# Performance work log

Measured on AMD Instinct MI355X. Metric: run time of the kernel, lower is better.

Reference implementation:

```python
import jax, jax.numpy as jnp
import numpy as np

SQ, SK, B, NP, HN = 2048, 2048, 2, 32, 64

def setup_inputs() -> dict:
    key = jax.random.key(0)
    kq, kk, kv, km = jax.random.split(key, 4)
    query = jax.random.normal(kq, (SQ, B, NP, HN), dtype=jnp.float32)
    k = jax.random.normal(kk, (SK, B, NP, HN), dtype=jnp.float32)
    value = jax.random.normal(kv, (SK, B, NP, HN), dtype=jnp.float32)
    # True = masked position (matches tf.where(mask, -10000.0, scores));
    # use a causal-style mask broadcast over heads.
    causal = ~jnp.tril(jnp.ones((SQ, SK), dtype=bool))  # True above diagonal
    attention_mask = jnp.broadcast_to(causal[None, None], (B, 1, SQ, SK))
    return {"query": query, "key": k, "value": value, "attention_mask": attention_mask}

def reference(query, key, value, attention_mask):
    sq, b, nh, hn = query.shape
    norm_factor = jnp.sqrt(jnp.asarray(hn, dtype=query.dtype))
    # scores: [b, nh, sq, sk]
    scores = jnp.einsum('sbnh,tbnh->bnst', query, key) / norm_factor
    scores = jnp.where(attention_mask, jnp.asarray(-10000.0, scores.dtype), scores)
    probs = jax.nn.softmax(scores, axis=-1)
    # dropout rate is 0.0 / inference -> identity
    # context: [sq, b, nh, hn] -> [sq, b, nh*hn]
    context = jnp.einsum('bnst,tbnh->sbnh', probs, value)
    return context.reshape(sq, b, nh * hn)
```

## Files before the change

### kernel.cpp

```cpp
#include <hip/hip_runtime.h>


typedef __attribute__((ext_vector_type(8))) short frag8;
typedef __attribute__((ext_vector_type(4))) float f32x4;
typedef __attribute__((ext_vector_type(2))) float f32x2;
typedef __attribute__((ext_vector_type(2))) __bf16 bf16x2;

#define SQ_    2048
#define NH_    64
#define HN_    64
#define ROWS_  4096
#define P_P    40
#define VT_P   40
#define TP_    72
#define SC2    (0.125f * 1.44269504088896340736f)
#define MASK2  (-3.0e4f)
#define MINIT  (-1.0e30f)

__device__ __forceinline__ unsigned short f2bf(float f) {
    unsigned u = __float_as_uint(f);
    u += 0x7fffu + ((u >> 16) & 1u);
    return (unsigned short)(u >> 16);
}

__device__ __forceinline__ float fexp2(float x) {
#if __has_builtin(__builtin_amdgcn_exp2f)
    return __builtin_amdgcn_exp2f(x);
#else
    return exp2f(x);
#endif
}

__device__ __forceinline__ unsigned pack_bf16x2(float lo, float hi) {
    bf16x2 h = __builtin_convertvector((f32x2){lo, hi}, bf16x2);
    unsigned r;
    __builtin_memcpy(&r, &h, 4);
    return r;
}

__device__ __forceinline__ frag8 pack8s(const float* __restrict__ p, float s) {
    float4 a = *(const float4*)p;
    float4 b = *(const float4*)(p + 4);
    frag8 r;
    r[0] = (short)f2bf(a.x * s); r[1] = (short)f2bf(a.y * s);
    r[2] = (short)f2bf(a.z * s); r[3] = (short)f2bf(a.w * s);
    r[4] = (short)f2bf(b.x * s); r[5] = (short)f2bf(b.y * s);
    r[6] = (short)f2bf(b.z * s); r[7] = (short)f2bf(b.w * s);
    return r;
}

__device__ __forceinline__ void gll(const void* g, void* l) {
    __builtin_amdgcn_global_load_lds(
        (const __attribute__((address_space(1))) unsigned int*)(uintptr_t)g,
        (__attribute__((address_space(3))) unsigned int*)(unsigned int)(uintptr_t)l,
        16, 0, 0);
}

__global__ void __launch_bounds__(256)
prep_kv(const float* __restrict__ K, const float* __restrict__ V,
        unsigned short* __restrict__ Kh, unsigned short* __restrict__ Vblk)
{
    __shared__ __align__(16) unsigned short tile[HN_ * TP_];
    const int tid = threadIdx.x;
    const int hd  = blockIdx.x & 63;
    const int s0  = (blockIdx.x >> 6) << 6;

    {
        const int c2 = tid & 3;
        const int sl = tid >> 2;
        const int s  = s0 + sl;
        const int sk = s >> 1;
        const float* kp = K + (size_t)s * ROWS_ + hd * HN_ + c2 * 16;
        frag8 A = pack8s(kp, 1.0f);
        frag8 Bf = pack8s(kp + 8, 1.0f);
        unsigned short* kr = Kh + (size_t)hd * (SQ_ * HN_) + (size_t)s * HN_;
        *(frag8*)(kr + ((2 * c2 + sk) & 7) * 8)     = A;
        *(frag8*)(kr + ((2 * c2 + 1 + sk) & 7) * 8) = Bf;
    }

    {
        const int c   = (tid & 15) * 4;
        const int tl0 = tid >> 4;
#pragma unroll
        for (int k = 0; k < 4; ++k) {
            const int tl = tl0 + k * 16;
            float4 v = *(const float4*)(V + (size_t)(s0 + tl) * ROWS_ + hd * HN_ + c);
            tile[(c + 0) * TP_ + tl] = f2bf(v.x);
            tile[(c + 1) * TP_ + tl] = f2bf(v.y);
            tile[(c + 2) * TP_ + tl] = f2bf(v.z);
            tile[(c + 3) * TP_ + tl] = f2bf(v.w);
        }
    }
    __syncthreads();
    {
        const int u  = tid & 3;
        const int dd = tid >> 2;
        const int rv = (dd + (dd >> 1)) & 3;
#pragma unroll
        for (int tb = 0; tb < 2; ++tb) {
            frag8 r = *(const frag8*)&tile[dd * TP_ + tb * 32 + u * 8];
            unsigned short* vr = Vblk + ((size_t)hd * 64 + (s0 >> 5) + tb) * 2048 + dd * 32;
            *(frag8*)(vr + ((u + rv) & 3) * 8) = r;
        }
    }
}

template <bool MASKED>
__device__ __forceinline__ void
ctile(const unsigned short* __restrict__ Kl, const unsigned short* __restrict__ Vl,
      int t0, int rowBase, int quad, int ln,
      const frag8& aq0, const frag8& aq1,
      unsigned short* __restrict__ PlW, f32x4 acc[4], float l_part[4])
{
    const int sw0 = ((quad + ln) & 7) * 8;
    const int sw1 = ((quad + 4 + ln) & 7) * 8;
    frag8 bk00 = *(const frag8*)(Kl + (2 * ln) * 64 + sw0);
    frag8 bk01 = *(const frag8*)(Kl + (2 * ln) * 64 + sw1);
    frag8 bk10 = *(const frag8*)(Kl + (2 * ln + 1) * 64 + sw0);
    frag8 bk11 = *(const frag8*)(Kl + (2 * ln + 1) * 64 + sw1);

    f32x4 c0 = (f32x4){0.f, 0.f, 0.f, 0.f};
    f32x4 c1 = (f32x4){0.f, 0.f, 0.f, 0.f};
    c0 = __builtin_amdgcn_mfma_f32_16x16x32_bf16(aq0, bk00, c0, 0, 0, 0);
    c0 = __builtin_amdgcn_mfma_f32_16x16x32_bf16(aq1, bk01, c0, 0, 0, 0);
    c1 = __builtin_amdgcn_mfma_f32_16x16x32_bf16(aq0, bk10, c1, 0, 0, 0);
    c1 = __builtin_amdgcn_mfma_f32_16x16x32_bf16(aq1, bk11, c1, 0, 0, 0);

#pragma unroll
    for (int r = 0; r < 4; ++r) {
        float p0 = fexp2(c0[r]);
        float p1 = fexp2(c1[r]);
        if (MASKED) {
            const int row = rowBase + quad * 4 + r;
            const int col = t0 + 2 * ln;
            p0 = (col > row)     ? 0.f : p0;
            p1 = (col + 1 > row) ? 0.f : p1;
        }
        l_part[r] += p0 + p1;
        *(unsigned*)&PlW[(quad * 4 + r) * P_P + 2 * ln] = pack_bf16x2(p0, p1);
    }

    const int rv = (ln + (ln >> 1)) & 3;
    const int swv = ((quad + rv) & 3) * 8;
    frag8 bv0 = *(const frag8*)(Vl + (0 * 16 + ln) * 32 + swv);
    frag8 bv1 = *(const frag8*)(Vl + (1 * 16 + ln) * 32 + swv);
    frag8 bv2 = *(const frag8*)(Vl + (2 * 16 + ln) * 32 + swv);
    frag8 bv3 = *(const frag8*)(Vl + (3 * 16 + ln) * 32 + swv);

    asm volatile("s_waitcnt lgkmcnt(0)" ::: "memory");
    frag8 ap = *(const frag8*)&PlW[ln * P_P + quad * 8];
    acc[0] = __builtin_amdgcn_mfma_f32_16x16x32_bf16(ap, bv0, acc[0], 0, 0, 0);
    acc[1] = __builtin_amdgcn_mfma_f32_16x16x32_bf16(ap, bv1, acc[1], 0, 0, 0);
    acc[2] = __builtin_amdgcn_mfma_f32_16x16x32_bf16(ap, bv2, acc[2], 0, 0, 0);
    acc[3] = __builtin_amdgcn_mfma_f32_16x16x32_bf16(ap, bv3, acc[3], 0, 0, 0);
}

__global__ void __launch_bounds__(256, 7)
attn_fwd3(const float* __restrict__ Qg,
          const unsigned short* __restrict__ Kh,
          const unsigned short* __restrict__ Vblk,
          float* __restrict__ Og)
{
    __shared__ __align__(16) unsigned short sbuf[2][4096];
    __shared__ __align__(16) unsigned short Pl[4][16 * P_P];

    const int tid  = threadIdx.x;
    const int wave = tid >> 6;
    const int lane = tid & 63;
    const int quad = lane >> 4;
    const int ln   = lane & 15;

    const int hd = blockIdx.x & 63;
    const int qt = 31 - (blockIdx.x >> 6);
    const int rowBase = qt * 64 + wave * 16;
    const int t0p  = rowBase & ~31;
    const int tiles = 2 * qt + 2;

    frag8 aq0, aq1;
    {
        const float* qp = Qg + (size_t)(rowBase + ln) * ROWS_ + hd * HN_ + quad * 8;
        aq0 = pack8s(qp, SC2);
        aq1 = pack8s(qp + 32, SC2);
    }

    f32x4 acc[4];
    float l_part[4];
#pragma unroll
    for (int r = 0; r < 4; ++r) {
        l_part[r] = 0.f;
        acc[r] = (f32x4){0.f, 0.f, 0.f, 0.f};
    }

    const unsigned short* khHead = Kh   + (size_t)hd * (SQ_ * HN_);
    const unsigned short* vbHead = Vblk + (size_t)hd * 64 * 2048;
    unsigned short* PlW = &Pl[wave][0];

    const int koff = (wave < 2) ? wave * 2048 : (wave - 2) * 2048;
    const int doff = (wave < 2) ? koff : 4096 + koff;

    {
        const char* src = (wave < 2) ? ((const char*)khHead) : ((const char*)vbHead);
        const char* s = src + koff + lane * 16;
        char* d = (char*)&sbuf[0][0] + doff;
        gll(s, d);
        gll(s + 1024, d + 1024);
    }

    for (int t = 0; t < tiles; ++t) {
        asm volatile("s_barrier" ::: "memory");
        {
            const int tn = (t + 1 < tiles) ? t + 1 : t;
            const char* src = (wave < 2) ? ((const char*)(khHead + (size_t)tn * 2048))
                                         : ((const char*)(vbHead + (size_t)tn * 2048));
            const char* s = src + koff + lane * 16;
            char* d = (char*)&sbuf[(t + 1) & 1][0] + doff;
            gll(s, d);
            gll(s + 1024, d + 1024);
        }
        asm volatile("s_waitcnt vmcnt(2)" ::: "memory");
        asm volatile("s_barrier" ::: "memory");

        const int t0 = t * 32;
        const unsigned short* Kl = &sbuf[t & 1][0];
        const unsigned short* Vl = &sbuf[t & 1][2048];
        if (t0 < t0p)
            ctile<false>(Kl, Vl, t0, rowBase, quad, ln, aq0, aq1, PlW, acc, l_part);
        else if (t0 == t0p)
            ctile<true>(Kl, Vl, t0, rowBase, quad, ln, aq0, aq1, PlW, acc, l_part);
    }
    asm volatile("s_waitcnt vmcnt(0)" ::: "memory");

#pragma unroll
    for (int r = 0; r < 4; ++r) {
        float l = l_part[r];
        l += __shfl_xor(l, 1);
        l += __shfl_xor(l, 2);
        l += __shfl_xor(l, 4);
        l += __shfl_xor(l, 8);
        const float inv = 1.0f / l;
        float* op = Og + (size_t)(rowBase + quad * 4 + r) * ROWS_ + hd * HN_ + ln;
        op[0]  = acc[0][r] * inv;
        op[16] = acc[1][r] * inv;
        op[32] = acc[2][r] * inv;
        op[48] = acc[3][r] * inv;
    }
}

__global__ void __launch_bounds__(256)
attn_fwd(const float* __restrict__ Qg, const float* __restrict__ Kg,
         const float* __restrict__ Vg, float* __restrict__ Og)
{
    __shared__ __align__(16) unsigned short Vt[HN_ * VT_P];
    __shared__ __align__(16) unsigned short Pl[4][16 * P_P];
    const int tid  = threadIdx.x;
    const int wave = tid >> 6;
    const int lane = tid & 63;
    const int quad = lane >> 4;
    const int ln   = lane & 15;
    const int hd = blockIdx.x % NH_;
    const int qt = 31 - (blockIdx.x / NH_);
    const int q0 = qt * 64;
    const int rowBase = q0 + wave * 16;
    frag8 aq0, aq1;
    {
        const float* qp = Qg + (size_t)(rowBase + ln) * ROWS_ + hd * HN_ + quad * 8;
        aq0 = pack8s(qp, 1.0f);
        aq1 = pack8s(qp + 32, 1.0f);
    }
    f32x4 acc[4];
    float m_i[4], l_i[4];
#pragma unroll
    for (int r = 0; r < 4; ++r) {
        m_i[r] = MINIT; l_i[r] = 0.f;
        acc[r] = (f32x4){0.f, 0.f, 0.f, 0.f};
    }
    const int tEnd = q0 + 64;
    for (int t0 = 0; t0 < tEnd; t0 += 32) {
        __syncthreads();
        {
            const int t  = tid >> 3;
            const int dc = tid & 7;
            const float* vp = Vg + (size_t)(t0 + t) * ROWS_ + hd * HN_ + dc * 8;
            float4 v0 = *(const float4*)vp;
            float4 v1 = *(const float4*)(vp + 4);
            Vt[(dc * 8 + 0) * VT_P + t] = f2bf(v0.x);
            Vt[(dc * 8 + 1) * VT_P + t] = f2bf(v0.y);
            Vt[(dc * 8 + 2) * VT_P + t] = f2bf(v0.z);
            Vt[(dc * 8 + 3) * VT_P + t] = f2bf(v0.w);
            Vt[(dc * 8 + 4) * VT_P + t] = f2bf(v1.x);
            Vt[(dc * 8 + 5) * VT_P + t] = f2bf(v1.y);
            Vt[(dc * 8 + 6) * VT_P + t] = f2bf(v1.z);
            Vt[(dc * 8 + 7) * VT_P + t] = f2bf(v1.w);
        }
        __syncthreads();
        float s0[4], s1[4];
#pragma unroll
        for (int sub = 0; sub < 2; ++sub) {
            const float* kp = Kg + (size_t)(t0 + sub * 16 + ln) * ROWS_ + hd * HN_ + quad * 8;
            frag8 bk0 = pack8s(kp, 1.0f);
            frag8 bk1 = pack8s(kp + 32, 1.0f);
            f32x4 c = (f32x4){0.f, 0.f, 0.f, 0.f};
            c = __builtin_amdgcn_mfma_f32_16x16x32_bf16(aq0, bk0, c, 0, 0, 0);
            c = __builtin_amdgcn_mfma_f32_16x16x32_bf16(aq1, bk1, c, 0, 0, 0);
            const int col = t0 + sub * 16 + ln;
            float* dst = sub ? s1 : s0;
#pragma unroll
            for (int r = 0; r < 4; ++r) {
                const int row = rowBase + quad * 4 + r;
                dst[r] = (col > row) ? MASK2 : c[r] * SC2;
            }
        }
#pragma unroll
        for (int r = 0; r < 4; ++r) {
            float mx = fmaxf(s0[r], s1[r]);
            mx = fmaxf(mx, __shfl_xor(mx, 1));
            mx = fmaxf(mx, __shfl_xor(mx, 2));
            mx = fmaxf(mx, __shfl_xor(mx, 4));
            mx = fmaxf(mx, __shfl_xor(mx, 8));
            const float mnew  = fmaxf(m_i[r], mx);
            const float alpha = fexp2(m_i[r] - mnew);
            const float p0 = fexp2(s0[r] - mnew);
            const float p1 = fexp2(s1[r] - mnew);
            float rs = p0 + p1;
            rs += __shfl_xor(rs, 1);
            rs += __shfl_xor(rs, 2);
            rs += __shfl_xor(rs, 4);
            rs += __shfl_xor(rs, 8);
            l_i[r] = l_i[r] * alpha + rs;
            m_i[r] = mnew;
#pragma unroll
            for (int dc = 0; dc < 4; ++dc) acc[dc][r] *= alpha;
            Pl[wave][(quad * 4 + r) * P_P + ln]      = f2bf(p0);
            Pl[wave][(quad * 4 + r) * P_P + 16 + ln] = f2bf(p1);
        }
        asm volatile("s_waitcnt lgkmcnt(0)" ::: "memory");
        frag8 ap = *(const frag8*)&Pl[wave][ln * P_P + quad * 8];
#pragma unroll
        for (int dc = 0; dc < 4; ++dc) {
            frag8 bv = *(const frag8*)&Vt[(dc * 16 + ln) * VT_P + quad * 8];
            acc[dc] = __builtin_amdgcn_mfma_f32_16x16x32_bf16(ap, bv, acc[dc], 0, 0, 0);
        }
    }
#pragma unroll
    for (int r = 0; r < 4; ++r) {
        const float inv = 1.0f / l_i[r];
        float* op = Og + (size_t)(rowBase + quad * 4 + r) * ROWS_ + hd * HN_ + ln;
#pragma unroll
        for (int dc = 0; dc < 4; ++dc)
            op[dc * 16] = acc[dc][r] * inv;
    }
}

extern "C" void kernel_launch(void* const* d_in, const int* in_sizes, int n_in,
                              void* d_out, int out_size, void* d_ws, size_t ws_size,
                              hipStream_t stream) {
    const float* Q = (const float*)d_in[0];
    const float* K = (const float*)d_in[1];
    const float* V = (const float*)d_in[2];
    float* O = (float*)d_out;

    const size_t HALF = (size_t)SQ_ * ROWS_ * sizeof(unsigned short);
    if (ws_size >= 2 * HALF) {
        unsigned short* Kh   = (unsigned short*)d_ws;
        unsigned short* Vblk = (unsigned short*)((char*)d_ws + HALF);
        prep_kv<<<dim3(NH_ * (SQ_ / 64)), dim3(256), 0, stream>>>(K, V, Kh, Vblk);
        attn_fwd3<<<dim3(2048), dim3(256), 0, stream>>>(Q, Kh, Vblk, O);
    } else {
        attn_fwd<<<dim3(2048), dim3(256), 0, stream>>>(Q, K, V, O);
    }
}
```

Baseline: 202.6 us.

## Process 32 query rows per wave with 128-row blocks to reuse K/V tiles

Each wave now handles two 16-row query groups (32 rows) against the same K/V fragments loaded from LDS, and each block covers 128 query rows, halving the grid to 1024 blocks. This halves global-to-LDS K/V traffic per query row and amortizes the K/V LDS reads over twice the MFMA work. In exchange it doubles the accumulator registers, lowers the occupancy target to 6 waves, and makes causal load imbalance coarser, since waves in a block now differ more in how many tiles they actually compute.

Result: slower. 654.2 us (+223.0%).

```diff
diff --git a/kernel.cpp b/kernel.cpp
--- a/kernel.cpp
+++ b/kernel.cpp
@@ -107,10 +107,10 @@
 
 template <bool MASKED>
 __device__ __forceinline__ void
-ctile(const unsigned short* __restrict__ Kl, const unsigned short* __restrict__ Vl,
-      int t0, int rowBase, int quad, int ln,
-      const frag8& aq0, const frag8& aq1,
-      unsigned short* __restrict__ PlW, f32x4 acc[4], float l_part[4])
+ctile32(const unsigned short* __restrict__ Kl, const unsigned short* __restrict__ Vl,
+        int t0, int rowBase, int quad, int ln,
+        const frag8 aq[2][2],
+        unsigned short* __restrict__ PlW, f32x4 acc[2][4], float l_part[2][4])
 {
     const int sw0 = ((quad + ln) & 7) * 8;
     const int sw1 = ((quad + 4 + ln) & 7) * 8;
@@ -119,25 +119,31 @@
     frag8 bk10 = *(const frag8*)(Kl + (2 * ln + 1) * 64 + sw0);
     frag8 bk11 = *(const frag8*)(Kl + (2 * ln + 1) * 64 + sw1);
 
-    f32x4 c0 = (f32x4){0.f, 0.f, 0.f, 0.f};
-    f32x4 c1 = (f32x4){0.f, 0.f, 0.f, 0.f};
-    c0 = __builtin_amdgcn_mfma_f32_16x16x32_bf16(aq0, bk00, c0, 0, 0, 0);
-    c0 = __builtin_amdgcn_mfma_f32_16x16x32_bf16(aq1, bk01, c0, 0, 0, 0);
-    c1 = __builtin_amdgcn_mfma_f32_16x16x32_bf16(aq0, bk10, c1, 0, 0, 0);
-    c1 = __builtin_amdgcn_mfma_f32_16x16x32_bf16(aq1, bk11, c1, 0, 0, 0);
-
-#pragma unroll
-    for (int r = 0; r < 4; ++r) {
-        float p0 = fexp2(c0[r]);
-        float p1 = fexp2(c1[r]);
+    f32x4 c[2][2];
+#pragma unroll
+    for (int g = 0; g < 2; ++g) {
+        c[g][0] = (f32x4){0.f, 0.f, 0.f, 0.f};
+        c[g][1] = (f32x4){0.f, 0.f, 0.f, 0.f};
+        c[g][0] = __builtin_amdgcn_mfma_f32_16x16x32_bf16(aq[g][0], bk00, c[g][0], 0, 0, 0);
+        c[g][0] = __builtin_amdgcn_mfma_f32_16x16x32_bf16(aq[g][1], bk01, c[g][0], 0, 0, 0);
+        c[g][1] = __builtin_amdgcn_mfma_f32_16x16x32_bf16(aq[g][0], bk10, c[g][1], 0, 0, 0);
+        c[g][1] = __builtin_amdgcn_mfma_f32_16x16x32_bf16(aq[g][1], bk11, c[g][1], 0, 0, 0);
+    }
+
+#pragma unroll
+    for (int g = 0; g < 2; ++g)
+#pragma unroll
+    for (int r = 0; r < 4; ++r) {
+        float p0 = fexp2(c[g][0][r]);
+        float p1 = fexp2(c[g][1][r]);
         if (MASKED) {
-            const int row = rowBase + quad * 4 + r;
+            const int row = rowBase + g * 16 + quad * 4 + r;
             const int col = t0 + 2 * ln;
             p0 = (col > row)     ? 0.f : p0;
             p1 = (col + 1 > row) ? 0.f : p1;
         }
-        l_part[r] += p0 + p1;
-        *(unsigned*)&PlW[(quad * 4 + r) * P_P + 2 * ln] = pack_bf16x2(p0, p1);
+        l_part[g][r] += p0 + p1;
+        *(unsigned*)&PlW[(g * 16 + quad * 4 + r) * P_P + 2 * ln] = pack_bf16x2(p0, p1);
     }
 
     const int rv = (ln + (ln >> 1)) & 3;
@@ -148,21 +154,24 @@
     frag8 bv3 = *(const frag8*)(Vl + (3 * 16 + ln) * 32 + swv);
 
     asm volatile("s_waitcnt lgkmcnt(0)" ::: "memory");
-    frag8 ap = *(const frag8*)&PlW[ln * P_P + quad * 8];
-    acc[0] = __builtin_amdgcn_mfma_f32_16x16x32_bf16(ap, bv0, acc[0], 0, 0, 0);
-    acc[1] = __builtin_amdgcn_mfma_f32_16x16x32_bf16(ap, bv1, acc[1], 0, 0, 0);
-    acc[2] = __builtin_amdgcn_mfma_f32_16x16x32_bf16(ap, bv2, acc[2], 0, 0, 0);
-    acc[3] = __builtin_amdgcn_mfma_f32_16x16x32_bf16(ap, bv3, acc[3], 0, 0, 0);
-}
-
-__global__ void __launch_bounds__(256, 7)
-attn_fwd3(const float* __restrict__ Qg,
+#pragma unroll
+    for (int g = 0; g < 2; ++g) {
+        frag8 ap = *(const frag8*)&PlW[(g * 16 + ln) * P_P + quad * 8];
+        acc[g][0] = __builtin_amdgcn_mfma_f32_16x16x32_bf16(ap, bv0, acc[g][0], 0, 0, 0);
+        acc[g][1] = __builtin_amdgcn_mfma_f32_16x16x32_bf16(ap, bv1, acc[g][1], 0, 0, 0);
+        acc[g][2] = __builtin_amdgcn_mfma_f32_16x16x32_bf16(ap, bv2, acc[g][2], 0, 0, 0);
+        acc[g][3] = __builtin_amdgcn_mfma_f32_16x16x32_bf16(ap, bv3, acc[g][3], 0, 0, 0);
+    }
+}
+
+__global__ void __launch_bounds__(256, 6)
+attn_fwd4(const float* __restrict__ Qg,
           const unsigned short* __restrict__ Kh,
           const unsigned short* __restrict__ Vblk,
           float* __restrict__ Og)
 {
     __shared__ __align__(16) unsigned short sbuf[2][4096];
-    __shared__ __align__(16) unsigned short Pl[4][16 * P_P];
+    __shared__ __align__(16) unsigned short Pl[4][32 * P_P];
 
     const int tid  = threadIdx.x;
     const int wave = tid >> 6;
@@ -170,25 +179,28 @@
     const int quad = lane >> 4;
     const int ln   = lane & 15;
 
-    const int hd = blockIdx.x & 63;
-    const int qt = 31 - (blockIdx.x >> 6);
-    const int rowBase = qt * 64 + wave * 16;
-    const int t0p  = rowBase & ~31;
-    const int tiles = 2 * qt + 2;
-
-    frag8 aq0, aq1;
-    {
-        const float* qp = Qg + (size_t)(rowBase + ln) * ROWS_ + hd * HN_ + quad * 8;
-        aq0 = pack8s(qp, SC2);
-        aq1 = pack8s(qp + 32, SC2);
-    }
-
-    f32x4 acc[4];
-    float l_part[4];
-#pragma unroll
-    for (int r = 0; r < 4; ++r) {
-        l_part[r] = 0.f;
-        acc[r] = (f32x4){0.f, 0.f, 0.f, 0.f};
+    const int hd  = blockIdx.x & 63;
+    const int qtb = 15 - (blockIdx.x >> 6);
+    const int rowBase = qtb * 128 + wave * 32;
+    const int tiles   = 4 * qtb + 4;
+    const int myTiles = (rowBase >> 5) + 1;
+
+    frag8 aq[2][2];
+#pragma unroll
+    for (int g = 0; g < 2; ++g) {
+        const float* qp = Qg + (size_t)(rowBase + g * 16 + ln) * ROWS_ + hd * HN_ + quad * 8;
+        aq[g][0] = pack8s(qp, SC2);
+        aq[g][1] = pack8s(qp + 32, SC2);
+    }
+
+    f32x4 acc[2][4];
+    float l_part[2][4];
+#pragma unroll
+    for (int g = 0; g < 2; ++g)
+#pragma unroll
+    for (int r = 0; r < 4; ++r) {
+        l_part[g][r] = 0.f;
+        acc[g][r] = (f32x4){0.f, 0.f, 0.f, 0.f};
     }
 
     const unsigned short* khHead = Kh   + (size_t)hd * (SQ_ * HN_);
@@ -223,26 +235,28 @@
         const int t0 = t * 32;
         const unsigned short* Kl = &sbuf[t & 1][0];
         const unsigned short* Vl = &sbuf[t & 1][2048];
-        if (t0 < t0p)
-            ctile<false>(Kl, Vl, t0, rowBase, quad, ln, aq0, aq1, PlW, acc, l_part);
-        else if (t0 == t0p)
-            ctile<true>(Kl, Vl, t0, rowBase, quad, ln, aq0, aq1, PlW, acc, l_part);
+        if (t + 1 < myTiles)
+            ctile32<false>(Kl, Vl, t0, rowBase, quad, ln, aq, PlW, acc, l_part);
+        else if (t + 1 == myTiles)
+            ctile32<true>(Kl, Vl, t0, rowBase, quad, ln, aq, PlW, acc, l_part);
     }
     asm volatile("s_waitcnt vmcnt(0)" ::: "memory");
 
 #pragma unroll
-    for (int r = 0; r < 4; ++r) {
-        float l = l_part[r];
+    for (int g = 0; g < 2; ++g)
+#pragma unroll
+    for (int r = 0; r < 4; ++r) {
+        float l = l_part[g][r];
         l += __shfl_xor(l, 1);
         l += __shfl_xor(l, 2);
         l += __shfl_xor(l, 4);
         l += __shfl_xor(l, 8);
         const float inv = 1.0f / l;
-        float* op = Og + (size_t)(rowBase + quad * 4 + r) * ROWS_ + hd * HN_ + ln;
-        op[0]  = acc[0][r] * inv;
-        op[16] = acc[1][r] * inv;
-        op[32] = acc[2][r] * inv;
-        op[48] = acc[3][r] * inv;
+        float* op = Og + (size_t)(rowBase + g * 16 + quad * 4 + r) * ROWS_ + hd * HN_ + ln;
+        op[0]  = acc[g][0][r] * inv;
+        op[16] = acc[g][1][r] * inv;
+        op[32] = acc[g][2][r] * inv;
+        op[48] = acc[g][3][r] * inv;
     }
 }
 
@@ -364,7 +378,7 @@
         unsigned short* Kh   = (unsigned short*)d_ws;
         unsigned short* Vblk = (unsigned short*)((char*)d_ws + HALF);
         prep_kv<<<dim3(NH_ * (SQ_ / 64)), dim3(256), 0, stream>>>(K, V, Kh, Vblk);
-        attn_fwd3<<<dim3(2048), dim3(256), 0, stream>>>(Q, Kh, Vblk, O);
+        attn_fwd4<<<dim3(NH_ * (SQ_ / 128)), dim3(256), 0, stream>>>(Q, Kh, Vblk, O);
     } else {
         attn_fwd<<<dim3(2048), dim3(256), 0, stream>>>(Q, K, V, O);
     }
```
